# Kernel optimization log

Measured on AMD Instinct MI355X. Metric: run time of the kernel, lower is better.

## Reference

```python
import jax, jax.numpy as jnp
import numpy as np

N_NODES = 50000
N_GRAPHS = 256
IN_DIM = 128
HID = 128
N_LAYERS = 3
N_EDGES = 800000


def setup_inputs() -> dict:
    key = jax.random.key(0)
    ks = jax.random.split(key, 16)
    x = jax.random.normal(ks[0], (N_NODES, IN_DIM), dtype=jnp.float32)
    edge_index = jax.random.randint(ks[1], (2, N_EDGES), 0, N_NODES, dtype=jnp.int64)
    batch = jnp.sort(jax.random.randint(ks[2], (N_NODES,), 0, N_GRAPHS, dtype=jnp.int64))
    inp = {"x": x, "edge_index": edge_index, "batch": batch}
    # SAGEConv params per PyG: lin_l (bias) applied to mean-aggregated neighbors,
    # lin_r (no bias) applied to the root node feature.
    dims = [(IN_DIM, HID)] + [(HID, HID)] * (N_LAYERS - 1)
    for i, (din, dout) in enumerate(dims):
        s = 1.0 / np.sqrt(din)
        inp[f"Wl{i}"] = jax.random.uniform(ks[3 + 3 * i], (din, dout), jnp.float32, -s, s)
        inp[f"bl{i}"] = jax.random.uniform(ks[4 + 3 * i], (dout,), jnp.float32, -s, s)
        inp[f"Wr{i}"] = jax.random.uniform(ks[5 + 3 * i], (din, dout), jnp.float32, -s, s)
    return inp


def _sage_conv(x, src, dst, Wl, bl, Wr):
    # mean aggregation of source-node messages into destination nodes
    msg = x[src]                                               # [E, d] gather
    agg = jax.ops.segment_sum(msg, dst, num_segments=N_NODES)  # [N, d] scatter-add
    deg = jax.ops.segment_sum(jnp.ones((src.shape[0], 1), x.dtype), dst,
                              num_segments=N_NODES)
    agg = agg / jnp.maximum(deg, 1.0)
    return agg @ Wl + bl + x @ Wr


def reference(x, edge_index, batch, Wl0, bl0, Wr0, Wl1, bl1, Wr1, Wl2, bl2, Wr2):
    src, dst = edge_index[0], edge_index[1]
    params = [(Wl0, bl0, Wr0), (Wl1, bl1, Wr1), (Wl2, bl2, Wr2)]
    h = x
    for Wl, bl, Wr in params:
        h = jax.nn.relu(_sage_conv(h, src, dst, Wl, bl, Wr))
        # dropout is a no-op in eval mode
    # meanmax readout over graph ids
    cnt = jax.ops.segment_sum(jnp.ones((h.shape[0], 1), h.dtype), batch,
                              num_segments=N_GRAPHS)
    g_mean = jax.ops.segment_sum(h, batch, num_segments=N_GRAPHS) / jnp.maximum(cnt, 1.0)
    g_max = jax.ops.segment_max(h, batch, num_segments=N_GRAPHS)
    g_max = jnp.where(jnp.isfinite(g_max), g_max, 0.0)  # empty graphs -> 0
    return jnp.concatenate([g_mean, g_max], axis=-1)    # [G, 2*HID]
```

## Files before the change

### kernel.cpp

```cpp
#include <hip/hip_runtime.h>
#include <hip/hip_bf16.h>
#include <stdint.h>

#define N_NODES  50000
#define N_GRAPHS 256
#define DIM      128
#define N_EDGES  800000
#define K2       256
#define N_STRIPS (N_NODES / 16)
#define PAD_CAP  64
#define NBUCKET  196
#define NCHUNK   256
#define CHUNK    3125

typedef __attribute__((ext_vector_type(8))) short  short8;
typedef __attribute__((ext_vector_type(4))) float  floatx4;

__device__ __forceinline__ ushort f2bf(float f) {
    union { float f; uint32_t u; } c; c.f = f;
    uint32_t u = c.u;
    return (ushort)((u + 0x7fffu + ((u >> 16) & 1u)) >> 16);
}
__device__ __forceinline__ float bf2f(ushort b) {
    union { uint32_t u; float f; } c; c.u = ((uint32_t)b) << 16;
    return c.f;
}

__global__ __launch_bounds__(256) void k_convert_x(const float* __restrict__ x,
                                                   ushort* __restrict__ xb) {
    int i = blockIdx.x * 256 + threadIdx.x;
    const int n4 = N_NODES * DIM / 4;
    if (i < n4) {
        float4 v = ((const float4*)x)[i];
        uint32_t lo = (uint32_t)f2bf(v.x) | ((uint32_t)f2bf(v.y) << 16);
        uint32_t hi = (uint32_t)f2bf(v.z) | ((uint32_t)f2bf(v.w) << 16);
        ((uint2*)xb)[i] = make_uint2(lo, hi);
    }
}

__global__ __launch_bounds__(256) void k_prep_w_all(const float* __restrict__ Wl0, const float* __restrict__ Wr0,
                                                    const float* __restrict__ Wl1, const float* __restrict__ Wr1,
                                                    const float* __restrict__ Wl2, const float* __restrict__ Wr2,
                                                    ushort* __restrict__ Wt) {
    int i = blockIdx.x * 256 + threadIdx.x;
    if (i < 3 * DIM * K2) {
        int layer = i / (DIM * K2);
        int j = i % (DIM * K2);
        int n = j / K2, k = j % K2;
        const float* Wl = (layer == 0) ? Wl0 : (layer == 1) ? Wl1 : Wl2;
        const float* Wr = (layer == 0) ? Wr0 : (layer == 1) ? Wr1 : Wr2;
        float v = (k < DIM) ? Wl[k * DIM + n] : Wr[(k - DIM) * DIM + n];
        Wt[i] = f2bf(v);
    }
}

__global__ __launch_bounds__(256) void k_hist(const int* __restrict__ dst,
                                              int* __restrict__ counts) {
    __shared__ int hist[NBUCKET];
    int t = threadIdx.x, b = blockIdx.x;
    if (t < NBUCKET) hist[t] = 0;
    __syncthreads();
    const int e0 = b * CHUNK;
    for (int i = t; i < CHUNK; i += 256)
        atomicAdd(&hist[dst[e0 + i] >> 8], 1);
    __syncthreads();
    if (t < NBUCKET) counts[b * NBUCKET + t] = hist[t];
}

__global__ __launch_bounds__(256) void k_scan_col(const int* __restrict__ counts,
                                                  int* __restrict__ off,
                                                  int* __restrict__ total) {
    __shared__ int buf[256];
    int t = threadIdx.x, j = blockIdx.x;
    int v = counts[t * NBUCKET + j];
    buf[t] = v;
    __syncthreads();
    #pragma unroll
    for (int d = 1; d < 256; d <<= 1) {
        int x = (t >= d) ? buf[t - d] : 0;
        __syncthreads();
        buf[t] += x;
        __syncthreads();
    }
    off[t * NBUCKET + j] = buf[t] - v;
    if (t == 255) total[j] = buf[255];
}

__global__ __launch_bounds__(256) void k_scan_total(const int* __restrict__ total,
                                                    int* __restrict__ basep) {
    __shared__ int buf[256];
    int t = threadIdx.x;
    int v = (t < NBUCKET) ? total[t] : 0;
    buf[t] = v;
    __syncthreads();
    #pragma unroll
    for (int d = 1; d < 256; d <<= 1) {
        int x = (t >= d) ? buf[t - d] : 0;
        __syncthreads();
        buf[t] += x;
        __syncthreads();
    }
    if (t < NBUCKET) basep[t] = buf[t] - v;
}

__global__ __launch_bounds__(256) void k_scatter(const int* __restrict__ src,
                                                 const int* __restrict__ dst,
                                                 const int* __restrict__ off,
                                                 const int* __restrict__ basep,
                                                 uint32_t* __restrict__ ebuf) {
    __shared__ int cur[NBUCKET];
    int t = threadIdx.x, b = blockIdx.x;
    if (t < NBUCKET) cur[t] = off[b * NBUCKET + t] + basep[t];
    __syncthreads();
    const int e0 = b * CHUNK;
    for (int i = t; i < CHUNK; i += 256) {
        int d = dst[e0 + i];
        int s = src[e0 + i];
        int p = atomicAdd(&cur[d >> 8], 1);
        ebuf[p] = ((uint32_t)(d & 255) << 16) | (uint32_t)s;
    }
}

__global__ __launch_bounds__(256) void k_build(const uint32_t* __restrict__ ebuf,
                                               const int* __restrict__ total,
                                               const int* __restrict__ basep,
                                               int* __restrict__ padded,
                                               int* __restrict__ cnt) {
    __shared__ int lcnt[256];
    int t = threadIdx.x, j = blockIdx.x;
    lcnt[t] = 0;
    __syncthreads();
    int b0 = basep[j], tot = total[j];
    for (int i = t; i < tot; i += 256) {
        uint32_t v = ebuf[b0 + i];
        int dl = (int)(v >> 16);
        int s  = (int)(v & 0xffffu);
        int p  = atomicAdd(&lcnt[dl], 1);
        if (p < PAD_CAP) padded[((size_t)j * 256 + dl) * PAD_CAP + p] = s;
    }
    __syncthreads();
    int node = j * 256 + t;
    if (node < N_NODES) cnt[node] = lcnt[t];
}

__global__ __launch_bounds__(256) void k_sort_adj(int* __restrict__ padded,
                                                  const int* __restrict__ cnt) {
    int wid  = threadIdx.x >> 6;
    int lane = threadIdx.x & 63;
    int node = blockIdx.x * 4 + wid;
    if (node >= N_NODES) return;
    int deg = cnt[node];
    int m   = deg < PAD_CAP ? deg : PAD_CAP;
    int* lst = padded + (size_t)node * PAD_CAP;
    int v = (lane < m) ? lst[lane] : 0x7fffffff;
    #pragma unroll
    for (int k = 2; k <= 64; k <<= 1) {
        #pragma unroll
        for (int j = k >> 1; j > 0; j >>= 1) {
            int other  = __shfl_xor(v, j, 64);
            bool down  = (lane & k) != 0;
            bool lower = (lane & j) == 0;
            v = (lower ^ down) ? min(v, other) : max(v, other);
        }
    }
    if (lane < m) lst[lane] = v;
}

__global__ __launch_bounds__(256) void k_gbounds(const int* __restrict__ batch,
                                                 int* __restrict__ gstart,
                                                 int* __restrict__ gend) {
    int i = blockIdx.x * 256 + threadIdx.x;
    if (i >= N_NODES) return;
    int g = batch[i];
    if (i == 0) gstart[g] = 0;
    int gn = (i + 1 < N_NODES) ? batch[i + 1] : -1;
    if (gn != g) {
        gend[g] = i + 1;
        if (gn >= 0) gstart[gn] = i + 1;
    }
}

template <bool OUT_F32>
__global__ __launch_bounds__(256) void k_layer(const ushort* __restrict__ h_in,
                                               const int* __restrict__ padded,
                                               const int* __restrict__ cnt,
                                               const ushort* __restrict__ Wt,
                                               const float* __restrict__ bias,
                                               ushort* __restrict__ out_bf,
                                               float* __restrict__ out_f) {
    __shared__ ushort sAgg[16 * DIM];
    int wid  = threadIdx.x >> 6;
    int lane = threadIdx.x & 63;
    int r0   = blockIdx.x * 16;
    const uint32_t* hw = (const uint32_t*)h_in;

    for (int q = 0; q < 4; ++q) {
        int node = r0 + wid * 4 + q;
        int deg = cnt[node];
        int m   = deg < PAD_CAP ? deg : PAD_CAP;
        const int* lst = padded + (size_t)node * PAD_CAP;
        float ax[4] = {0.f, 0.f, 0.f, 0.f};
        float ay[4] = {0.f, 0.f, 0.f, 0.f};
        for (int e = 0; e < m; e += 16) {
            int idx[16];
            uint32_t v[16];
            #pragma unroll
            for (int k = 0; k < 16; ++k) {
                int ek = e + k;
                idx[k] = lst[ek < m ? ek : m - 1];
            }
            #pragma unroll
            for (int k = 0; k < 16; ++k)
                v[k] = hw[(size_t)idx[k] * 64 + lane];
            #pragma unroll
            for (int k = 0; k < 16; ++k) {
                uint32_t w = (e + k < m) ? v[k] : 0u;
                ax[k & 3] += bf2f((ushort)(w & 0xffffu));
                ay[k & 3] += bf2f((ushort)(w >> 16));
            }
        }
        float axs = (ax[0] + ax[1]) + (ax[2] + ax[3]);
        float ays = (ay[0] + ay[1]) + (ay[2] + ay[3]);
        float inv = 1.0f / (float)(deg > 0 ? deg : 1);
        uint32_t o = (uint32_t)f2bf(axs * inv) | ((uint32_t)f2bf(ays * inv) << 16);
        ((uint32_t*)(sAgg + (wid * 4 + q) * DIM))[lane] = o;
    }
    __syncthreads();

    int row  = lane & 15;
    int quad = lane >> 4;
    short8 a[8];
    const ushort* srow = sAgg + row * DIM + quad * 8;
    #pragma unroll
    for (int ks = 0; ks < 4; ++ks) a[ks] = *(const short8*)(srow + ks * 32);
    const ushort* hrow = h_in + (size_t)(r0 + row) * DIM + quad * 8;
    #pragma unroll
    for (int ks = 0; ks < 4; ++ks) a[4 + ks] = *(const short8*)(hrow + ks * 32);

    #pragma unroll
    for (int c = 0; c < 2; ++c) {
        int ct  = wid * 2 + c;
        int col = ct * 16 + row;
        const ushort* wrow = Wt + (size_t)col * K2 + quad * 8;
        floatx4 acc = {0.f, 0.f, 0.f, 0.f};
        #pragma unroll
        for (int ks = 0; ks < 8; ++ks) {
            short8 b = *(const short8*)(wrow + ks * 32);
            acc = __builtin_amdgcn_mfma_f32_16x16x32_bf16(a[ks], b, acc, 0, 0, 0);
        }
        float bv = bias[col];
        #pragma unroll
        for (int r = 0; r < 4; ++r) {
            int m = r0 + quad * 4 + r;
            float v = acc[r] + bv;
            v = v > 0.f ? v : 0.f;
            if (OUT_F32) out_f[(size_t)m * DIM + col] = v;
            else         out_bf[(size_t)m * DIM + col] = f2bf(v);
        }
    }
}

__global__ __launch_bounds__(128) void k_readout(const float* __restrict__ h,
                                                 const int* __restrict__ batch,
                                                 float* __restrict__ out) {
    int d  = threadIdx.x;
    int n0 = blockIdx.x * 128;
    int n1 = min(n0 + 128, N_NODES);
    int cur = -1; float sum = 0.f, mx = 0.f;
    for (int i = n0; i < n1; ++i) {
        int g = batch[i];
        if (g != cur) {
            if (cur >= 0) {
                atomicAdd(&out[cur * 2 * DIM + d], sum);
                atomicMax((int*)&out[cur * 2 * DIM + DIM + d], __float_as_int(mx));
            }
            cur = g; sum = 0.f; mx = 0.f;
        }
        float v = h[(size_t)i * DIM + d];
        sum += v; mx = fmaxf(mx, v);
    }
    if (cur >= 0) {
        atomicAdd(&out[cur * 2 * DIM + d], sum);
        atomicMax((int*)&out[cur * 2 * DIM + DIM + d], __float_as_int(mx));
    }
}

__global__ __launch_bounds__(256) void k_finalize(float* __restrict__ out,
                                                  const int* __restrict__ gstart,
                                                  const int* __restrict__ gend) {
    int i = blockIdx.x * 256 + threadIdx.x;
    if (i < N_GRAPHS * DIM) {
        int g = i / DIM, d = i % DIM;
        int c = gend[g] - gstart[g];
        out[g * 2 * DIM + d] /= (float)(c > 0 ? c : 1);
    }
}

extern "C" void kernel_launch(void* const* d_in, const int* in_sizes, int n_in,
                              void* d_out, int out_size, void* d_ws, size_t ws_size,
                              hipStream_t stream) {
    const float* x     = (const float*)d_in[0];
    const int*   ei    = (const int*)d_in[1];
    const int*   src   = ei;
    const int*   dst   = ei + N_EDGES;
    const int*   batch = (const int*)d_in[2];
    const float* Wl[3] = {(const float*)d_in[3], (const float*)d_in[6], (const float*)d_in[9]};
    const float* bl[3] = {(const float*)d_in[4], (const float*)d_in[7], (const float*)d_in[10]};
    const float* Wr[3] = {(const float*)d_in[5], (const float*)d_in[8], (const float*)d_in[11]};
    float* out = (float*)d_out;

    char* base = (char*)d_ws;
    size_t o = 0;
    auto alloc = [&](size_t b) -> char* {
        char* p = base + o;
        o = (o + b + 255) & ~(size_t)255;
        return p;
    };
    int*     gstart = (int*)alloc((size_t)N_GRAPHS * 4);
    int*     gend   = (int*)alloc((size_t)N_GRAPHS * 4);
    size_t   zero_bytes = o;
    int*     cnt    = (int*)alloc((size_t)N_NODES * 4);
    int*     counts = (int*)alloc((size_t)NCHUNK * NBUCKET * 4);
    int*     offs   = (int*)alloc((size_t)NCHUNK * NBUCKET * 4);
    int*     total  = (int*)alloc((size_t)NBUCKET * 4);
    int*     basep  = (int*)alloc((size_t)NBUCKET * 4);
    uint32_t* ebuf  = (uint32_t*)alloc((size_t)N_EDGES * 4);
    int*     padded = (int*)alloc((size_t)N_NODES * PAD_CAP * 4);
    ushort*  xb     = (ushort*)alloc((size_t)N_NODES * DIM * 2);
    ushort*  ha     = (ushort*)alloc((size_t)N_NODES * DIM * 2);
    ushort*  hb     = (ushort*)alloc((size_t)N_NODES * DIM * 2);
    float*   h3     = (float*)alloc((size_t)N_NODES * DIM * 4);
    ushort*  Wt     = (ushort*)alloc((size_t)3 * DIM * K2 * 2);
    (void)ws_size; (void)n_in; (void)in_sizes;

    hipMemsetAsync(base, 0, zero_bytes, stream);
    hipMemsetAsync(d_out, 0, (size_t)out_size * 4, stream);

    k_convert_x<<<(N_NODES * DIM / 4 + 255) / 256, 256, 0, stream>>>(x, xb);
    k_prep_w_all<<<(3 * DIM * K2 + 255) / 256, 256, 0, stream>>>(
        Wl[0], Wr[0], Wl[1], Wr[1], Wl[2], Wr[2], Wt);

    k_hist<<<NCHUNK, 256, 0, stream>>>(dst, counts);
    k_scan_col<<<NBUCKET, 256, 0, stream>>>(counts, offs, total);
    k_scan_total<<<1, 256, 0, stream>>>(total, basep);
    k_scatter<<<NCHUNK, 256, 0, stream>>>(src, dst, offs, basep, ebuf);
    k_build<<<NBUCKET, 256, 0, stream>>>(ebuf, total, basep, padded, cnt);
    k_sort_adj<<<(N_NODES + 3) / 4, 256, 0, stream>>>(padded, cnt);
    k_gbounds<<<(N_NODES + 255) / 256, 256, 0, stream>>>(batch, gstart, gend);

    k_layer<false><<<N_STRIPS, 256, 0, stream>>>(xb, padded, cnt, Wt,              bl[0], ha, nullptr);
    k_layer<false><<<N_STRIPS, 256, 0, stream>>>(ha, padded, cnt, Wt + DIM * K2,   bl[1], hb, nullptr);
    k_layer<true ><<<N_STRIPS, 256, 0, stream>>>(hb, padded, cnt, Wt + 2 * DIM * K2, bl[2], nullptr, h3);

    k_readout<<<(N_NODES + 127) / 128, 128, 0, stream>>>(h3, batch, out);
    k_finalize<<<(N_GRAPHS * DIM + 255) / 256, 256, 0, stream>>>(out, gstart, gend);
}
```

Measured before the change: 365.2 us.

## Stage neighbor lists in LDS and double-buffer gather chunks across nodes

Each block now loads its 16 nodes' padded neighbor lists and degrees into shared memory up front. Each wave builds a flat list of 16-edge chunks spanning its four nodes. A two-register-buffer software pipeline then issues the next chunk's gathers while accumulating the current one. This hides global gather latency across node boundaries and removes dependent index loads from global memory, at the cost of more registers and LDS, which may reduce occupancy. The bf16-to-float conversion is also simplified to a shift and mask.

```diff
diff --git a/kernel.cpp b/kernel.cpp
--- a/kernel.cpp
+++ b/kernel.cpp
@@ -189,41 +189,93 @@
                                                ushort* __restrict__ out_bf,
                                                float* __restrict__ out_f) {
     __shared__ ushort sAgg[16 * DIM];
-    int wid  = threadIdx.x >> 6;
-    int lane = threadIdx.x & 63;
+    __shared__ int    sIdx[16 * PAD_CAP];
+    __shared__ int    sCnt[16];
+    __shared__ int    sChl[4][17];
+    __shared__ int    sNch[4];
+
+    int t    = threadIdx.x;
+    int wid  = t >> 6;
+    int lane = t & 63;
     int r0   = blockIdx.x * 16;
     const uint32_t* hw = (const uint32_t*)h_in;
 
+    ((int4*)sIdx)[t] = ((const int4*)(padded + (size_t)r0 * PAD_CAP))[t];
+    if (t < 16) sCnt[t] = cnt[r0 + t];
+    __syncthreads();
+
+    if (lane == 0) {
+        int n = 0;
+        #pragma unroll
+        for (int q = 0; q < 4; ++q) {
+            int m = min(sCnt[wid * 4 + q], PAD_CAP);
+            for (int e0 = 0; e0 < m; e0 += 16)
+                sChl[wid][n++] = q | (e0 << 8);
+        }
+        sNch[wid] = n;
+    }
+    #pragma unroll
     for (int q = 0; q < 4; ++q) {
-        int node = r0 + wid * 4 + q;
-        int deg = cnt[node];
-        int m   = deg < PAD_CAP ? deg : PAD_CAP;
-        const int* lst = padded + (size_t)node * PAD_CAP;
-        float ax[4] = {0.f, 0.f, 0.f, 0.f};
-        float ay[4] = {0.f, 0.f, 0.f, 0.f};
-        for (int e = 0; e < m; e += 16) {
-            int idx[16];
-            uint32_t v[16];
+        int node = wid * 4 + q;
+        if (sCnt[node] == 0) ((uint32_t*)(sAgg + node * DIM))[lane] = 0u;
+    }
+    int nch = sNch[wid];
+
+    float ax[4] = {0.f, 0.f, 0.f, 0.f};
+    float ay[4] = {0.f, 0.f, 0.f, 0.f};
+    uint32_t va[16], vb[16];
+
+    auto issue = [&](int ci, uint32_t (&v)[16]) {
+        int ch   = sChl[wid][ci];
+        int q    = ch & 255, e0 = ch >> 8;
+        int node = wid * 4 + q;
+        int m    = min(sCnt[node], PAD_CAP);
+        const int* lst = sIdx + node * PAD_CAP;
+        #pragma unroll
+        for (int k = 0; k < 16; ++k) {
+            int ek = e0 + k;
+            int id = lst[ek < m ? ek : m - 1];
+            v[k] = hw[(size_t)id * 64 + lane];
+        }
+    };
+    auto consume = [&](int ci, uint32_t (&v)[16], bool isLast) {
+        int ch   = sChl[wid][ci];
+        int q    = ch & 255, e0 = ch >> 8;
+        int node = wid * 4 + q;
+        int deg  = sCnt[node];
+        int m    = min(deg, PAD_CAP);
+        #pragma unroll
+        for (int k = 0; k < 16; ++k) {
+            uint32_t w = (e0 + k < m) ? v[k] : 0u;
+            ax[k & 3] += __uint_as_float(w << 16);
+            ay[k & 3] += __uint_as_float(w & 0xffff0000u);
+        }
+        bool lastOfNode = isLast || ((sChl[wid][ci + 1] & 255) != q);
+        if (lastOfNode) {
+            float axs = (ax[0] + ax[1]) + (ax[2] + ax[3]);
+            float ays = (ay[0] + ay[1]) + (ay[2] + ay[3]);
+            float inv = 1.0f / (float)(deg > 0 ? deg : 1);
+            uint32_t o = (uint32_t)f2bf(axs * inv) | ((uint32_t)f2bf(ays * inv) << 16);
+            ((uint32_t*)(sAgg + node * DIM))[lane] = o;
             #pragma unroll
-            for (int k = 0; k < 16; ++k) {
-                int ek = e + k;
-                idx[k] = lst[ek < m ? ek : m - 1];
-            }
-            #pragma unroll
-            for (int k = 0; k < 16; ++k)
-                v[k] = hw[(size_t)idx[k] * 64 + lane];
-            #pragma unroll
-            for (int k = 0; k < 16; ++k) {
-                uint32_t w = (e + k < m) ? v[k] : 0u;
-                ax[k & 3] += bf2f((ushort)(w & 0xffffu));
-                ay[k & 3] += bf2f((ushort)(w >> 16));
-            }
-        }
-        float axs = (ax[0] + ax[1]) + (ax[2] + ax[3]);
-        float ays = (ay[0] + ay[1]) + (ay[2] + ay[3]);
-        float inv = 1.0f / (float)(deg > 0 ? deg : 1);
-        uint32_t o = (uint32_t)f2bf(axs * inv) | ((uint32_t)f2bf(ays * inv) << 16);
-        ((uint32_t*)(sAgg + (wid * 4 + q) * DIM))[lane] = o;
+            for (int j = 0; j < 4; ++j) { ax[j] = 0.f; ay[j] = 0.f; }
+        }
+    };
+
+    if (nch > 0) {
+        issue(0, va);
+        int i = 0;
+        while (true) {
+            bool hasB = (i + 1) < nch;
+            if (hasB) issue(i + 1, vb);
+            consume(i, va, !hasB);
+            if (!hasB) break;
+            bool hasA = (i + 2) < nch;
+            if (hasA) issue(i + 2, va);
+            consume(i + 1, vb, !hasA);
+            if (!hasA) break;
+            i += 2;
+        }
     }
     __syncthreads();
 
```

Measured after the change: 348.0 us. -4.7%, faster.
